# Performance work log

Measured on AMD Instinct MI355X. Metric: run time of the kernel, lower is better.

Reference implementation:

```python
import jax, jax.numpy as jnp
import numpy as np

R_SPHERE = 3.0   # bounding_sphere_radius
NEAR = 0.0       # near_distance
FAR = 100.0      # far_distance
SECANT_STEPS = 4 # manifold_secant_steps
EPS = 1e-4
R0 = 1.0         # base radius of analytic manifold field


def setup_inputs() -> dict:
    key = jax.random.key(0)
    ks = jax.random.split(key, 6)
    B, R, L, H = 4, 8192, 4, 64
    rays_o = jax.random.normal(ks[0], (B, R, 3), dtype=jnp.float32) * 0.2  # origins inside sphere
    rd = jax.random.normal(ks[1], (B, R, 3), dtype=jnp.float32)
    rays_d = rd / jnp.linalg.norm(rd, axis=-1, keepdims=True)
    levels = jnp.linspace(0.5, -0.5, L, dtype=jnp.float32)  # manifold_levels parameter
    W1 = jax.random.normal(ks[2], (3, H), dtype=jnp.float32) * 0.3
    b1 = jnp.zeros((H,), dtype=jnp.float32)
    W2 = jax.random.normal(ks[3], (H, 1), dtype=jnp.float32) * 0.1
    b2 = jnp.zeros((1,), dtype=jnp.float32)
    rays_idx = jax.random.randint(ks[4], (B, R), 0, B, dtype=jnp.int64) if jax.config.jax_enable_x64 else jax.random.randint(ks[4], (B, R), 0, B, dtype=jnp.int32)
    mask_gt = jnp.ones((B, R), dtype=bool)
    return {"rays_o": rays_o, "rays_d": rays_d, "levels": levels, "W1": W1, "b1": b1,
            "W2": W2, "b2": b2, "mask_gt": mask_gt, "rays_idx": rays_idx, "num_samples": 64}


def _ray_march(rays_o, rays_d, levels, W1, b1, W2, b2, num_samples):
    B, Rn = rays_o.shape[:2]
    N = B * Rn
    L = levels.shape[0]
    o = rays_o.reshape(N, 3)
    d = rays_d.reshape(N, 3)

    def manifold_fn(x):
        # analytic stand-in for M(x_d, idx): scalar field + validity mask
        h = jnp.tanh(x @ W1 + b1)
        nrm = jnp.linalg.norm(x, axis=-1)
        s = (h @ W2)[..., 0] + b2[0] + (R0 - nrm)
        return s, nrm < R_SPHERE

    # ray-sphere intersection (unit-norm directions assumed, as in source)
    b = jnp.sum(o * d, axis=-1)
    c = jnp.sum(o * o, axis=-1) - R_SPHERE ** 2
    disc = b * b - c
    hit = disc > 0
    sq = jnp.sqrt(jnp.where(hit, disc, 1.0))
    d_near = jnp.maximum(-b - sq, NEAR)
    d_far = jnp.minimum(-b + sq, FAR)
    mask_bound = hit & (d_near < d_far)

    # stratified (uniform) depth samples, (N, S)
    t = jnp.linspace(0.0, 1.0, num_samples, dtype=rays_o.dtype)[None, :]
    ds = d_near[:, None] * (1 - t) + d_far[:, None] * t
    x_d = o[:, None, :] + d[:, None, :] * ds[..., None]  # (N, S, 3)
    scal, m_valid = manifold_fn(x_d)                      # (N, S)

    # --- find_closest_interval ---
    S = num_samples
    dep_f, dep_b = ds[:, :-1], ds[:, 1:]
    sc_f, sc_b = scal[:, :-1], scal[:, 1:]
    m_pair = m_valid[:, :-1] & m_valid[:, 1:]
    l3 = levels[None, :, None]                            # (1, L, 1)
    in_interval = (sc_f[:, None, :] >= l3) & (l3 >= sc_b[:, None, :]) & m_pair[:, None, :]
    rank = jnp.sign(l3 - sc_b[:, None, :]) * jnp.arange(S - 1, 0, -1, dtype=scal.dtype)
    ind_closest = jnp.argmax(rank, axis=2)                # (N, L)
    ind_lowest = jnp.broadcast_to(jnp.argmin(sc_b, axis=1)[:, None], (N, L))
    mask_surface = jnp.any(in_interval, axis=2)
    idx = jnp.where(mask_surface, ind_closest, ind_lowest)
    d_front = jnp.take_along_axis(dep_f, idx, axis=1)
    d_back = jnp.take_along_axis(dep_b, idx, axis=1)
    s_front = jnp.take_along_axis(sc_f, idx, axis=1)
    s_back = jnp.take_along_axis(sc_b, idx, axis=1)

    # --- find_exact_intersection ---
    lr = levels[None, :]                                  # (1, L)
    s_diff = s_front - s_back
    m_vdiff = jnp.abs(s_diff) > EPS
    mask_intersect = (s_front >= lr) & (lr >= s_back)
    mask_secant = mask_intersect & m_vdiff
    s_diff_safe = jnp.where(m_vdiff, s_diff, 1.0)
    d_secant = ((lr - s_back) * d_front + (s_front - lr) * d_back) / s_diff_safe
    d_init = jnp.where(mask_secant, d_secant, d_back)

    # secant refinement (fixed step count; masked full-array updates replace
    # torch's boolean-indexed subset updates with identical math on masked lanes)
    dfs, dbs, sfs, sbs, dcur = d_front, d_back, s_front, s_back, d_init
    for _ in range(SECANT_STEPS):
        x_mid = o[:, None, :] + dcur[..., None] * d[:, None, :]  # (N, L, 3)
        s_mid, mv = manifold_fn(x_mid)
        upf = (s_mid > lr) & mv
        upb = (s_mid < lr) & mv
        dfs = jnp.where(upf, dcur, dfs)
        sfs = jnp.where(upf, s_mid, sfs)
        dbs = jnp.where(upb, dcur, dbs)
        sbs = jnp.where(upb, s_mid, sbs)
        sd = sfs - sbs
        ok = jnp.abs(sd) > EPS
        dcur = jnp.where(ok, ((lr - sbs) * dfs + (sfs - lr) * dbs) / jnp.where(ok, sd, 1.0), dcur)
    d_intersect = jnp.where(mask_secant, dcur, d_init)

    # sort intersections by depth (use_presort=False branch)
    order = jnp.argsort(d_intersect, axis=1)
    d_intersect = jnp.take_along_axis(d_intersect, order, axis=1)
    mask_intersect = jnp.take_along_axis(mask_intersect, order, axis=1)

    dist = jnp.where(mask_bound[:, None], d_intersect, 0.0).reshape(B, Rn, L)
    mask = (mask_intersect & mask_bound[:, None]).reshape(B, Rn, L)
    return dist, mask


def reference(rays_o, rays_d, levels, W1, b1, W2, b2, mask_gt, rays_idx, num_samples):
    # mask_gt / rays_idx are unused in eval mode (use_gt_mask_when_training=False,
    # analytic manifold_fn ignores batch index), kept for signature fidelity.
    return _ray_march(rays_o, rays_d, levels, W1, b1, W2, b2, num_samples)
```

## Files before the change

### kernel.cpp

```cpp
#include <hip/hip_runtime.h>
#include <cstdint>

#define R_SPHEREf 3.0f
#define NEARf 0.0f
#define FARf 100.0f
#define SECANT_STEPS 4
#define EPSf 1e-4f
#define R0f 1.0f
#define Hh 64
#define Lc 4
#define Sn 64

#define C_HI 2.88539004325866699f
#define C_LO 3.8519227871e-08f

__global__ __launch_bounds__(256) void manifold_render_kernel(
    const float* __restrict__ rays_o, const float* __restrict__ rays_d,
    const float* __restrict__ levels, const float* __restrict__ W1,
    const float* __restrict__ b1, const float* __restrict__ W2,
    const float* __restrict__ b2, float* __restrict__ out, int N)
{
    __shared__ float4 abq[4][Hh];

    const int tid = threadIdx.x;
    const int wave = tid >> 6;
    const int lane = tid & 63;
    const int r = blockIdx.x * 4 + wave;
    const bool ray_ok = (r < N);

    const float b2v = b2[0];
    float lvl[Lc];
#pragma unroll
    for (int j = 0; j < Lc; ++j) lvl[j] = levels[j];

    float ox = 0.f, oy = 0.f, oz = 0.f, dx = 0.f, dy = 0.f, dz = 1.f;
    if (ray_ok) {
        ox = rays_o[3 * r]; oy = rays_o[3 * r + 1]; oz = rays_o[3 * r + 2];
        dx = rays_d[3 * r]; dy = rays_d[3 * r + 1]; dz = rays_d[3 * r + 2];
    }

    float w2lane;
    {
        const float w1x = W1[lane], w1y = W1[Hh + lane], w1z = W1[2 * Hh + lane];
        w2lane = W2[lane];
        const float Ah = __builtin_fmaf(oz, w1z, __builtin_fmaf(oy, w1y,
                         __builtin_fmaf(ox, w1x, b1[lane])));
        const float Bh = __builtin_fmaf(dz, w1z, __builtin_fmaf(dy, w1y, dx * w1x));
        const float A2 = __builtin_fmaf(Ah, C_LO, Ah * C_HI);
        const float B2 = __builtin_fmaf(Bh, C_LO, Bh * C_HI);
        abq[wave][lane] = make_float4(A2, B2, -2.0f * w2lane, 0.0f);
    }
    float w2sum = w2lane;
#pragma unroll
    for (int m = 1; m < 64; m <<= 1) w2sum += __shfl_xor(w2sum, m);
    const float sbase = w2sum + b2v + R0f;

    __syncthreads();
    if (!ray_ok) return;

    const float bq = ox * dx + oy * dy + oz * dz;
    const float cq = ox * ox + oy * oy + oz * oz - R_SPHEREf * R_SPHEREf;
    const float disc = bq * bq - cq;
    const bool hit = disc > 0.0f;
    const float sq = sqrtf(hit ? disc : 1.0f);
    const float d_near = fmaxf(-bq - sq, NEARf);
    const float d_far  = fminf(-bq + sq, FARf);
    const bool mask_bound = hit && (d_near < d_far);

    const float t = (float)lane / (float)(Sn - 1);
    const float dsv = d_near * (1.0f - t) + d_far * t;
    const float x0 = ox + dx * dsv, x1 = oy + dy * dsv, x2 = oz + dz * dsv;
    const float nrm = sqrtf(x0 * x0 + x1 * x1 + x2 * x2);

    const float4* __restrict__ ab = &abq[wave][0];
    float acc = 0.0f;
#pragma unroll
    for (int h = 0; h < Hh; ++h) {
        const float4 q = ab[h];
        const float y = __builtin_fmaf(dsv, q.y, q.x);
        const float e = __builtin_amdgcn_exp2f(y);
        const float r1 = __builtin_amdgcn_rcpf(e + 1.0f);
        acc = __builtin_fmaf(q.z, r1, acc);
    }
    const float scal = (acc + sbase) - nrm;
    const bool valid = nrm < R_SPHEREf;

    const float scb = __shfl_down(scal, 1);
    const int validn = __shfl_down((int)valid, 1);
    const bool is_int = lane < (Sn - 1);

    float keyv = is_int ? scb : INFINITY;
    int keyi = lane;
#pragma unroll
    for (int m = 1; m < 64; m <<= 1) {
        float ov = __shfl_xor(keyv, m);
        int oi = __shfl_xor(keyi, m);
        if (ov < keyv || (ov == keyv && oi < keyi)) { keyv = ov; keyi = oi; }
    }
    const int ind_lowest = keyi;

    const bool inint_base = is_int && valid && (validn != 0);

    bool mintb[Lc], msec[Lc];
    float dinit[Lc];
    float g_dfs = 0.f, g_dbs = 0.f, g_sfs = 0.f, g_sbs = 0.f, g_dcur = 0.f, g_lr = 0.f;
    const int g = lane >> 4;

#pragma unroll
    for (int lv = 0; lv < Lc; ++lv) {
        const float l = lvl[lv];
        unsigned long long bP = __ballot(is_int && (scb < l));
        unsigned long long bZ = __ballot(is_int && (scb == l));
        unsigned long long bI = __ballot(inint_base && (scal >= l) && (l >= scb));
        int ind_closest = bP ? __builtin_ctzll(bP)
                             : (bZ ? __builtin_ctzll(bZ) : (Sn - 2));
        bool mask_surface = (bI != 0ULL);
        int idx = mask_surface ? ind_closest : ind_lowest;

        float d_front = __shfl(dsv, idx);
        float d_back  = __shfl(dsv, idx + 1);
        float s_front = __shfl(scal, idx);
        float s_back  = __shfl(scal, idx + 1);

        bool mi = (s_front >= l) && (l >= s_back);
        float sd = s_front - s_back;
        bool vd = fabsf(sd) > EPSf;
        bool ms = mi && vd;
        float d_sec = ((l - s_back) * d_front + (s_front - l) * d_back) / (vd ? sd : 1.0f);
        float di = ms ? d_sec : d_back;

        mintb[lv] = mi; msec[lv] = ms; dinit[lv] = di;
        if (g == lv) {
            g_dfs = d_front; g_dbs = d_back; g_sfs = s_front; g_sbs = s_back;
            g_dcur = di; g_lr = l;
        }
    }

    const int sub = lane & 15;
    float4 sq0 = ab[sub], sq1 = ab[sub + 16], sq2 = ab[sub + 32], sq3 = ab[sub + 48];

#pragma unroll
    for (int it = 0; it < SECANT_STEPS; ++it) {
        float mx0 = ox + g_dcur * dx, mx1 = oy + g_dcur * dy, mx2 = oz + g_dcur * dz;
        float mn = sqrtf(mx0 * mx0 + mx1 * mx1 + mx2 * mx2);
        float part;
        {
            float y0 = __builtin_fmaf(g_dcur, sq0.y, sq0.x);
            float y1 = __builtin_fmaf(g_dcur, sq1.y, sq1.x);
            float y2 = __builtin_fmaf(g_dcur, sq2.y, sq2.x);
            float y3 = __builtin_fmaf(g_dcur, sq3.y, sq3.x);
            float r0 = __builtin_amdgcn_rcpf(__builtin_amdgcn_exp2f(y0) + 1.0f);
            float r1 = __builtin_amdgcn_rcpf(__builtin_amdgcn_exp2f(y1) + 1.0f);
            float r2 = __builtin_amdgcn_rcpf(__builtin_amdgcn_exp2f(y2) + 1.0f);
            float r3 = __builtin_amdgcn_rcpf(__builtin_amdgcn_exp2f(y3) + 1.0f);
            part = sq0.z * r0;
            part = __builtin_fmaf(sq1.z, r1, part);
            part = __builtin_fmaf(sq2.z, r2, part);
            part = __builtin_fmaf(sq3.z, r3, part);
        }
#pragma unroll
        for (int m = 1; m < 16; m <<= 1) part += __shfl_xor(part, m, 16);
        float s_mid = (part + sbase) - mn;
        bool mv = mn < R_SPHEREf;
        bool upf = (s_mid > g_lr) && mv;
        bool upb = (s_mid < g_lr) && mv;
        if (upf) { g_dfs = g_dcur; g_sfs = s_mid; }
        if (upb) { g_dbs = g_dcur; g_sbs = s_mid; }
        float sd2 = g_sfs - g_sbs;
        bool ok = fabsf(sd2) > EPSf;
        if (ok) g_dcur = ((g_lr - g_sbs) * g_dfs + (g_sfs - g_lr) * g_dbs) / sd2;
    }

    float v0, v1, v2, v3;
    {
        float dc0 = __shfl(g_dcur, 0);
        float dc1 = __shfl(g_dcur, 16);
        float dc2 = __shfl(g_dcur, 32);
        float dc3 = __shfl(g_dcur, 48);
        v0 = msec[0] ? dc0 : dinit[0];
        v1 = msec[1] ? dc1 : dinit[1];
        v2 = msec[2] ? dc2 : dinit[2];
        v3 = msec[3] ? dc3 : dinit[3];
    }
    int m0 = mintb[0], m1 = mintb[1], m2 = mintb[2], m3 = mintb[3];
    int i0 = 0, i1 = 1, i2 = 2, i3 = 3;

#define CSWAP(va, ia, ma, vb, ib, mb)                                    \
    { bool sw = (vb < va) || (vb == va && ib < ia);                      \
      if (sw) { float tv = va; va = vb; vb = tv;                         \
                int ti = ia; ia = ib; ib = ti;                           \
                int tm = ma; ma = mb; mb = tm; } }
    CSWAP(v0, i0, m0, v1, i1, m1);
    CSWAP(v2, i2, m2, v3, i3, m3);
    CSWAP(v0, i0, m0, v2, i2, m2);
    CSWAP(v1, i1, m1, v3, i3, m3);
    CSWAP(v1, i1, m1, v2, i2, m2);
#undef CSWAP

    const long long NL = (long long)N * Lc;
    if (lane < Lc) {
        float dv = (lane == 0) ? v0 : (lane == 1) ? v1 : (lane == 2) ? v2 : v3;
        out[(long long)r * Lc + lane] = mask_bound ? dv : 0.0f;
    } else if (lane < 2 * Lc) {
        int k = lane - Lc;
        int mm = (k == 0) ? m0 : (k == 1) ? m1 : (k == 2) ? m2 : m3;
        out[NL + (long long)r * Lc + k] = (mm && mask_bound) ? 1.0f : 0.0f;
    }
}

extern "C" void kernel_launch(void* const* d_in, const int* in_sizes, int n_in,
                              void* d_out, int out_size, void* d_ws, size_t ws_size,
                              hipStream_t stream) {
    const float* rays_o = (const float*)d_in[0];
    const float* rays_d = (const float*)d_in[1];
    const float* levels = (const float*)d_in[2];
    const float* W1 = (const float*)d_in[3];
    const float* b1 = (const float*)d_in[4];
    const float* W2 = (const float*)d_in[5];
    const float* b2 = (const float*)d_in[6];
    float* out = (float*)d_out;

    const int N = in_sizes[0] / 3;
    const int blocks = (N + 3) / 4;
    manifold_render_kernel<<<blocks, 256, 0, stream>>>(
        rays_o, rays_d, levels, W1, b1, W2, b2, out, N);
}
```

Baseline: 129.4 us.

## Evaluate MLP samples via geometric exp recurrence and LDS transpose reduction

Replaces the per-sample loop over 64 hidden units (one exp2 and one rcp each) with a per-hidden-unit recurrence along the uniformly spaced samples. exp(B*d) advances by a constant factor per step, so each lane computes one hidden unit's sigmoid terms for all 64 samples with only an rcp and an fma per sample. The terms go into a padded LDS buffer and are summed transposed per sample in two halves. It also swaps IEEE division and sqrt for rcp with one Newton step and the hardware sqrt. The cost is a large per-wave shared buffer that may lower occupancy, plus recurrence error that can build up or overflow for large exponents and may flip marginal interval decisions.

After: 129.7 us. About the same (+0.2%).

```diff
diff --git a/kernel.cpp b/kernel.cpp
--- a/kernel.cpp
+++ b/kernel.cpp
@@ -14,6 +14,12 @@
 #define C_HI 2.88539004325866699f
 #define C_LO 3.8519227871e-08f
 
+__device__ __forceinline__ float fastdiv(float a, float b) {
+    float r = __builtin_amdgcn_rcpf(b);
+    r = __builtin_fmaf(r, __builtin_fmaf(-b, r, 1.0f), r);
+    return a * r;
+}
+
 __global__ __launch_bounds__(256) void manifold_render_kernel(
     const float* __restrict__ rays_o, const float* __restrict__ rays_d,
     const float* __restrict__ levels, const float* __restrict__ W1,
@@ -21,67 +27,98 @@
     const float* __restrict__ b2, float* __restrict__ out, int N)
 {
     __shared__ float4 abq[4][Hh];
+    __shared__ float Pbuf[4][Hh][33];
 
     const int tid = threadIdx.x;
     const int wave = tid >> 6;
     const int lane = tid & 63;
     const int r = blockIdx.x * 4 + wave;
-    const bool ray_ok = (r < N);
+    if (r >= N) return;
 
     const float b2v = b2[0];
     float lvl[Lc];
 #pragma unroll
     for (int j = 0; j < Lc; ++j) lvl[j] = levels[j];
 
-    float ox = 0.f, oy = 0.f, oz = 0.f, dx = 0.f, dy = 0.f, dz = 1.f;
-    if (ray_ok) {
-        ox = rays_o[3 * r]; oy = rays_o[3 * r + 1]; oz = rays_o[3 * r + 2];
-        dx = rays_d[3 * r]; dy = rays_d[3 * r + 1]; dz = rays_d[3 * r + 2];
-    }
-
-    float w2lane;
-    {
-        const float w1x = W1[lane], w1y = W1[Hh + lane], w1z = W1[2 * Hh + lane];
-        w2lane = W2[lane];
-        const float Ah = __builtin_fmaf(oz, w1z, __builtin_fmaf(oy, w1y,
-                         __builtin_fmaf(ox, w1x, b1[lane])));
-        const float Bh = __builtin_fmaf(dz, w1z, __builtin_fmaf(dy, w1y, dx * w1x));
-        const float A2 = __builtin_fmaf(Ah, C_LO, Ah * C_HI);
-        const float B2 = __builtin_fmaf(Bh, C_LO, Bh * C_HI);
-        abq[wave][lane] = make_float4(A2, B2, -2.0f * w2lane, 0.0f);
-    }
+    const float ox = rays_o[3 * r], oy = rays_o[3 * r + 1], oz = rays_o[3 * r + 2];
+    const float dx = rays_d[3 * r], dy = rays_d[3 * r + 1], dz = rays_d[3 * r + 2];
+
+    const float w1x = W1[lane], w1y = W1[Hh + lane], w1z = W1[2 * Hh + lane];
+    const float w2lane = W2[lane];
+    const float Ah = __builtin_fmaf(oz, w1z, __builtin_fmaf(oy, w1y,
+                     __builtin_fmaf(ox, w1x, b1[lane])));
+    const float Bh = __builtin_fmaf(dz, w1z, __builtin_fmaf(dy, w1y, dx * w1x));
+    const float A2 = __builtin_fmaf(Ah, C_LO, Ah * C_HI);
+    const float B2 = __builtin_fmaf(Bh, C_LO, Bh * C_HI);
+    const float zq = -2.0f * w2lane;
+    abq[wave][lane] = make_float4(A2, B2, zq, 0.0f);
+
     float w2sum = w2lane;
 #pragma unroll
     for (int m = 1; m < 64; m <<= 1) w2sum += __shfl_xor(w2sum, m);
     const float sbase = w2sum + b2v + R0f;
-
-    __syncthreads();
-    if (!ray_ok) return;
 
     const float bq = ox * dx + oy * dy + oz * dz;
     const float cq = ox * ox + oy * oy + oz * oz - R_SPHEREf * R_SPHEREf;
     const float disc = bq * bq - cq;
     const bool hit = disc > 0.0f;
-    const float sq = sqrtf(hit ? disc : 1.0f);
-    const float d_near = fmaxf(-bq - sq, NEARf);
-    const float d_far  = fminf(-bq + sq, FARf);
+    const float sqv = __builtin_amdgcn_sqrtf(hit ? disc : 1.0f);
+    const float d_near = fmaxf(-bq - sqv, NEARf);
+    const float d_far  = fminf(-bq + sqv, FARf);
     const bool mask_bound = hit && (d_near < d_far);
 
-    const float t = (float)lane / (float)(Sn - 1);
+    const float delta = (d_far - d_near) * (1.0f / 63.0f);
+    const float zs = copysignf(fmaxf(fabsf(zq), 1e-30f), zq);
+    float rz = __builtin_amdgcn_rcpf(zs);
+    rz = __builtin_fmaf(rz, __builtin_fmaf(-zs, rz, 1.0f), rz);
+    const float e0 = __builtin_amdgcn_exp2f(__builtin_fmaf(d_near, B2, A2));
+    const float g  = __builtin_amdgcn_exp2f(B2 * delta);
+    const float cc = (1.0f - g) * rz;
+    float u = __builtin_fmaf(e0, rz, rz);
+
+    float* __restrict__ Pw = &Pbuf[wave][0][0];
+    const int sl = lane & 31;
+    float accA, accB;
+
+#pragma unroll
+    for (int s = 0; s < 32; ++s) {
+        Pw[lane * 33 + s] = __builtin_amdgcn_rcpf(u);
+        u = __builtin_fmaf(u, g, cc);
+    }
+    {
+        float a0 = 0.f, a1 = 0.f, a2 = 0.f, a3 = 0.f;
+#pragma unroll
+        for (int h = 0; h < Hh; h += 4) {
+            a0 += Pw[(h    ) * 33 + sl];
+            a1 += Pw[(h + 1) * 33 + sl];
+            a2 += Pw[(h + 2) * 33 + sl];
+            a3 += Pw[(h + 3) * 33 + sl];
+        }
+        accA = (a0 + a1) + (a2 + a3);
+    }
+    asm volatile("s_waitcnt lgkmcnt(0)" ::: "memory");
+#pragma unroll
+    for (int s = 0; s < 32; ++s) {
+        Pw[lane * 33 + s] = __builtin_amdgcn_rcpf(u);
+        u = __builtin_fmaf(u, g, cc);
+    }
+    {
+        float a0 = 0.f, a1 = 0.f, a2 = 0.f, a3 = 0.f;
+#pragma unroll
+        for (int h = 0; h < Hh; h += 4) {
+            a0 += Pw[(h    ) * 33 + sl];
+            a1 += Pw[(h + 1) * 33 + sl];
+            a2 += Pw[(h + 2) * 33 + sl];
+            a3 += Pw[(h + 3) * 33 + sl];
+        }
+        accB = (a0 + a1) + (a2 + a3);
+    }
+    const float acc = (lane < 32) ? accA : accB;
+
+    const float t = (float)lane * (1.0f / 63.0f);
     const float dsv = d_near * (1.0f - t) + d_far * t;
     const float x0 = ox + dx * dsv, x1 = oy + dy * dsv, x2 = oz + dz * dsv;
-    const float nrm = sqrtf(x0 * x0 + x1 * x1 + x2 * x2);
-
-    const float4* __restrict__ ab = &abq[wave][0];
-    float acc = 0.0f;
-#pragma unroll
-    for (int h = 0; h < Hh; ++h) {
-        const float4 q = ab[h];
-        const float y = __builtin_fmaf(dsv, q.y, q.x);
-        const float e = __builtin_amdgcn_exp2f(y);
-        const float r1 = __builtin_amdgcn_rcpf(e + 1.0f);
-        acc = __builtin_fmaf(q.z, r1, acc);
-    }
+    const float nrm = __builtin_amdgcn_sqrtf(x0 * x0 + x1 * x1 + x2 * x2);
     const float scal = (acc + sbase) - nrm;
     const bool valid = nrm < R_SPHEREf;
 
@@ -104,7 +141,7 @@
     bool mintb[Lc], msec[Lc];
     float dinit[Lc];
     float g_dfs = 0.f, g_dbs = 0.f, g_sfs = 0.f, g_sbs = 0.f, g_dcur = 0.f, g_lr = 0.f;
-    const int g = lane >> 4;
+    const int gl = lane >> 4;
 
 #pragma unroll
     for (int lv = 0; lv < Lc; ++lv) {
@@ -126,23 +163,25 @@
         float sd = s_front - s_back;
         bool vd = fabsf(sd) > EPSf;
         bool ms = mi && vd;
-        float d_sec = ((l - s_back) * d_front + (s_front - l) * d_back) / (vd ? sd : 1.0f);
+        float d_sec = fastdiv((l - s_back) * d_front + (s_front - l) * d_back,
+                              vd ? sd : 1.0f);
         float di = ms ? d_sec : d_back;
 
         mintb[lv] = mi; msec[lv] = ms; dinit[lv] = di;
-        if (g == lv) {
+        if (gl == lv) {
             g_dfs = d_front; g_dbs = d_back; g_sfs = s_front; g_sbs = s_back;
             g_dcur = di; g_lr = l;
         }
     }
 
+    const float4* __restrict__ ab = &abq[wave][0];
     const int sub = lane & 15;
     float4 sq0 = ab[sub], sq1 = ab[sub + 16], sq2 = ab[sub + 32], sq3 = ab[sub + 48];
 
 #pragma unroll
     for (int it = 0; it < SECANT_STEPS; ++it) {
         float mx0 = ox + g_dcur * dx, mx1 = oy + g_dcur * dy, mx2 = oz + g_dcur * dz;
-        float mn = sqrtf(mx0 * mx0 + mx1 * mx1 + mx2 * mx2);
+        float mn = __builtin_amdgcn_sqrtf(mx0 * mx0 + mx1 * mx1 + mx2 * mx2);
         float part;
         {
             float y0 = __builtin_fmaf(g_dcur, sq0.y, sq0.x);
@@ -168,7 +207,7 @@
         if (upb) { g_dbs = g_dcur; g_sbs = s_mid; }
         float sd2 = g_sfs - g_sbs;
         bool ok = fabsf(sd2) > EPSf;
-        if (ok) g_dcur = ((g_lr - g_sbs) * g_dfs + (g_sfs - g_lr) * g_dbs) / sd2;
+        if (ok) g_dcur = fastdiv((g_lr - g_sbs) * g_dfs + (g_sfs - g_lr) * g_dbs, sd2);
     }
 
     float v0, v1, v2, v3;
```
